# Optimization experiments

Measured on AMD Instinct MI355X. Metric: run time of the kernel, lower is better.

Reference implementation:

```python
import jax, jax.numpy as jnp
import numpy as np

N_HEAD, N_KV, HD, CA_DIM, VE_CH = 16, 4, 64, 32, 12
B, T, C = 4, 1024, 1024
FFN_H = 4 * C
CA_STEPS = 4

def rms_norm(x):
    return x * jax.lax.rsqrt(jnp.mean(x * x, axis=-1, keepdims=True) + 1e-6)

def rope(x, cos, sin):
    d = x.shape[-1] // 2
    x1, x2 = x[..., :d], x[..., d:]
    return jnp.concatenate([x1 * cos + x2 * sin, -x1 * sin + x2 * cos], axis=-1)

def dwconv1d(x_bct, w, pad):  # w: (Cch,1,K) depthwise
    return jax.lax.conv_general_dilated(x_bct, w, (1,), [(pad, pad)],
        feature_group_count=x_bct.shape[1], dimension_numbers=('NCH', 'OIH', 'NCH'))

def dwconv2d(x_bchw, w):  # w: (Cch,1,3,3) depthwise
    return jax.lax.conv_general_dilated(x_bchw, w, (1, 1), [(1, 1), (1, 1)],
        feature_group_count=x_bchw.shape[1], dimension_numbers=('NCHW', 'OIHW', 'NCHW'))

def ca_channel(x, ca_pi, ca_cw, ca_po):
    h = x @ ca_pi.T  # (B,T,CA_DIM)
    h = h + 0.1 * jnp.transpose(dwconv1d(jnp.transpose(h, (0, 2, 1)), ca_cw, 1), (0, 2, 1))
    return jax.nn.gelu(h, approximate=False) @ ca_po.T

def setup_inputs() -> dict:
    key = jax.random.key(0)
    ks = jax.random.split(key, 20)
    s = 0.02
    pos = jnp.arange(T, dtype=jnp.float32)
    inv_freq = 1.0 / (10000.0 ** (jnp.arange(HD // 2, dtype=jnp.float32) / (HD // 2)))
    ang = pos[:, None] * inv_freq[None, :]  # (T, HD/2)
    return {
        'x': jax.random.normal(ks[0], (B, T, C), jnp.float32),
        've': jax.random.normal(ks[1], (B, T, N_KV * HD), jnp.float32),
        'cos': jnp.cos(ang)[None, :, None, :],
        'sin': jnp.sin(ang)[None, :, None, :],
        'prev_attn': jax.random.uniform(ks[2], (B, N_HEAD, T, T), jnp.float32),
        'w_q': s * jax.random.normal(ks[3], (N_HEAD * HD, C), jnp.float32),
        'w_k': s * jax.random.normal(ks[4], (N_KV * HD, C), jnp.float32),
        'w_v': s * jax.random.normal(ks[5], (N_KV * HD, C), jnp.float32),
        'w_o': s * jax.random.normal(ks[6], (C, C), jnp.float32),
        'w_ve_gate': s * jax.random.normal(ks[7], (N_KV, VE_CH), jnp.float32),
        'refine_w': s * jax.random.normal(ks[8], (N_HEAD, 1, 3, 3), jnp.float32),
        'refine_alpha': jnp.float32(0.05),
        'ca_pi': s * jax.random.normal(ks[9], (CA_DIM, C), jnp.float32),
        'ca_cw': s * jax.random.normal(ks[10], (CA_DIM, 1, 3), jnp.float32),
        'ca_po': s * jax.random.normal(ks[11], (C, CA_DIM), jnp.float32),
        'ffn_in': s * jax.random.normal(ks[12], (FFN_H, C), jnp.float32),
        'ffn_cw': s * jax.random.normal(ks[13], (FFN_H, 1, 3), jnp.float32),
        'ffn_out': s * jax.random.normal(ks[14], (C, FFN_H), jnp.float32),
        'ffn_gate': s * jax.random.normal(ks[15], (C, C), jnp.float32),
        'vit_w1': s * jax.random.normal(ks[16], (32, C), jnp.float32),
        'vit_w2': s * jax.random.normal(ks[17], (1, 32), jnp.float32),
    }

def reference(x, ve, cos, sin, prev_attn, w_q, w_k, w_v, w_o, w_ve_gate,
              refine_w, refine_alpha, ca_pi, ca_cw, ca_po,
              ffn_in, ffn_cw, ffn_out, ffn_gate, vit_w1, vit_w2):
    Bx, Tx, Cx = x.shape
    xn = rms_norm(x)
    q = (xn @ w_q.T).reshape(Bx, Tx, N_HEAD, HD)
    k = (xn @ w_k.T).reshape(Bx, Tx, N_KV, HD)
    v = (xn @ w_v.T).reshape(Bx, Tx, N_KV, HD)
    gate = 3.0 * jax.nn.sigmoid(xn[..., :VE_CH] @ w_ve_gate.T)  # (B,T,N_KV)
    v = v + gate[..., None] * ve.reshape(Bx, Tx, N_KV, HD)
    q = rms_norm(rope(q, cos, sin)) * 1.2
    k = rms_norm(rope(k, cos, sin)) * 1.2
    r = N_HEAD // N_KV
    k = jnp.repeat(k, r, axis=2)
    v = jnp.repeat(v, r, axis=2)
    q, k, v = (jnp.transpose(t, (0, 2, 1, 3)) for t in (q, k, v))  # (B,H,T,HD)
    att = jnp.einsum('bhqd,bhkd->bhqk', q, k) * (1.0 / np.sqrt(HD))
    att = att + refine_alpha * dwconv2d(prev_attn[:, :, :Tx, :Tx], refine_w)
    cmask = jnp.tril(jnp.ones((Tx, Tx), bool))
    att = jnp.where(cmask, att, -jnp.inf)
    aw = jax.nn.softmax(att, axis=-1)
    y = jnp.einsum('bhqk,bhkd->bhqd', aw, v)
    attn_out = jnp.transpose(y, (0, 2, 1, 3)).reshape(Bx, Tx, Cx) @ w_o.T
    # ca_mode='both': gate the attention output
    ca1 = ca_channel(x, ca_pi, ca_cw, ca_po)
    x1 = x + attn_out * (1.0 + 0.1 * jnp.tanh(ca1))
    # CAFFN
    xm = rms_norm(x1)
    h = jnp.square(jax.nn.relu(xm @ ffn_in.T))  # (B,T,FFN_H)
    ht = jnp.transpose(h, (0, 2, 1))
    for _ in range(CA_STEPS):
        ht = ht + 0.1 * dwconv1d(ht, ffn_cw, 1)
    h = jnp.transpose(ht, (0, 2, 1))
    mlp = (h @ ffn_out.T) * jax.nn.sigmoid(xm @ ffn_gate.T)
    ca2 = ca_channel(x1, ca_pi, ca_cw, ca_po)
    mlp = mlp * (1.0 + 0.1 * jnp.tanh(ca2))
    # vitality gating: MLP -> sigmoid, then avg_pool1d(k=5, pad=2, zero-counted)
    vit = jax.nn.sigmoid(jax.nn.gelu(x1 @ vit_w1.T, approximate=False) @ vit_w2.T)[..., 0]  # (B,T)
    vp = jnp.pad(vit, ((0, 0), (2, 2)))
    vs = sum(vp[:, i:i + Tx] for i in range(5)) / 5.0
    vit = 0.7 * vit + 0.3 * vs
    vit = jnp.where(vit > 0.3, vit, vit * 0.1)
    return x1 + mlp * vit[..., None]
```

## Files before the change

kernel.cpp:

```cpp
#include <hip/hip_runtime.h>

#define BB 4
#define TT 1024
#define CC 1024
#define NH 16
#define NKV 4
#define HD 64
#define FFNH 4096
#define CAD 32
#define TQ 64
#define TK 64

typedef short bf16x8 __attribute__((ext_vector_type(8)));
typedef float f32x4  __attribute__((ext_vector_type(4)));

#define AS1 __attribute__((address_space(1)))
#define AS3 __attribute__((address_space(3)))

__device__ __forceinline__ float sigf(float x){ return 1.f/(1.f+__expf(-x)); }
__device__ __forceinline__ float geluf(float x){ return 0.5f*x*(1.f+erff(x*0.70710678118654752f)); }

__device__ __forceinline__ unsigned short f2bf(float f){
  unsigned int u = __float_as_uint(f);
  u += 0x7fffu + ((u >> 16) & 1u);
  return (unsigned short)(u >> 16);
}
__device__ __forceinline__ float bf2f(unsigned short h){
  return __uint_as_float(((unsigned int)h) << 16);
}

__global__ __launch_bounds__(256) void rmsnorm_pair_k(const float* __restrict__ x,
    unsigned short* __restrict__ oh, unsigned short* __restrict__ ol){
  int row = blockIdx.x;
  const float* xr = x + (size_t)row * CC;
  float v[4]; float ss = 0.f;
  #pragma unroll
  for (int i = 0; i < 4; i++){ v[i] = xr[threadIdx.x + 256*i]; ss += v[i]*v[i]; }
  #pragma unroll
  for (int off = 1; off < 64; off <<= 1) ss += __shfl_xor(ss, off);
  __shared__ float red[4];
  if ((threadIdx.x & 63) == 0) red[threadIdx.x >> 6] = ss;
  __syncthreads();
  float tot = red[0]+red[1]+red[2]+red[3];
  float rs = rsqrtf(tot * (1.f/CC) + 1e-6f);
  size_t base = (size_t)row * CC;
  #pragma unroll
  for (int i = 0; i < 4; i++){
    float r = v[i]*rs;
    unsigned short h = f2bf(r);
    oh[base + threadIdx.x + 256*i] = h;
    ol[base + threadIdx.x + 256*i] = f2bf(r - bf2f(h));
  }
}

__global__ __launch_bounds__(256) void split_k(const float* __restrict__ in,
    unsigned short* __restrict__ hi, unsigned short* __restrict__ lo, int n4){
  int i = blockIdx.x*256 + threadIdx.x;
  if (i >= n4) return;
  float4 v = ((const float4*)in)[i];
  unsigned short h0 = f2bf(v.x), h1 = f2bf(v.y), h2v = f2bf(v.z), h3 = f2bf(v.w);
  ushort4 hv = { h0, h1, h2v, h3 };
  ushort4 lv = { f2bf(v.x - bf2f(h0)), f2bf(v.y - bf2f(h1)),
                 f2bf(v.z - bf2f(h2v)), f2bf(v.w - bf2f(h3)) };
  ((ushort4*)hi)[i] = hv;
  ((ushort4*)lo)[i] = lv;
}

template<int EPI>
__global__ __launch_bounds__(256) void gemm3_k(
    const unsigned short* __restrict__ Ah, const unsigned short* __restrict__ Al,
    const unsigned short* __restrict__ Wh, const unsigned short* __restrict__ Wl,
    float* __restrict__ C, int M, int N, int K)
{
  __shared__ unsigned short AhS[128*32];
  __shared__ unsigned short AlS[128*32];
  __shared__ unsigned short WhS[128*32];
  __shared__ unsigned short WlS[128*32];
  int tid  = threadIdx.x;
  int lane = tid & 63, wave = tid >> 6;
  int wr = wave >> 1, wc = wave & 1;
  int m0 = blockIdx.y << 7, n0 = blockIdx.x << 7;
  int lr = lane & 15, lc = lane >> 4;

  int offA[4], offB[4];
  #pragma unroll
  for (int m = 0; m < 4; m++){
    int row = wr*64 + m*16 + lr;
    offA[m] = row*64 + ((lc ^ ((row >> 1) & 3)) << 4);
  }
  #pragma unroll
  for (int n = 0; n < 4; n++){
    int row = wc*64 + n*16 + lr;
    offB[n] = row*64 + ((lc ^ ((row >> 1) & 3)) << 4);
  }

  f32x4 acc[4][4] = {};

  for (int k0 = 0; k0 < K; k0 += 32){
    __syncthreads();
    {
      const unsigned short* srcs[4] = { Ah, Al, Wh, Wl };
      unsigned short* dsts[4] = { AhS, AlS, WhS, WlS };
      int rb[4] = { m0, m0, n0, n0 };
      #pragma unroll
      for (int tle = 0; tle < 4; tle++){
        #pragma unroll
        for (int i = 0; i < 2; i++){
          int s = i*256 + tid;
          int row = s >> 2;
          int c = (s & 3) ^ ((row >> 1) & 3);
          const unsigned short* gp = srcs[tle] + (size_t)(rb[tle] + row)*K + (k0 + c*8);
          unsigned short* lp = dsts[tle] + i*2048 + wave*512;
          __builtin_amdgcn_global_load_lds((const AS1 void*)gp, (AS3 void*)lp, 16, 0, 0);
        }
      }
    }
    __syncthreads();

    bf16x8 ah[4], al[4], bh[4], bl[4];
    #pragma unroll
    for (int m = 0; m < 4; m++){
      ah[m] = *(const bf16x8*)((const char*)AhS + offA[m]);
      al[m] = *(const bf16x8*)((const char*)AlS + offA[m]);
    }
    #pragma unroll
    for (int n = 0; n < 4; n++){
      bh[n] = *(const bf16x8*)((const char*)WhS + offB[n]);
      bl[n] = *(const bf16x8*)((const char*)WlS + offB[n]);
    }
    #pragma unroll
    for (int m = 0; m < 4; m++){
      #pragma unroll
      for (int n = 0; n < 4; n++){
        acc[m][n] = __builtin_amdgcn_mfma_f32_16x16x32_bf16(al[m], bh[n], acc[m][n], 0, 0, 0);
        acc[m][n] = __builtin_amdgcn_mfma_f32_16x16x32_bf16(ah[m], bl[n], acc[m][n], 0, 0, 0);
        acc[m][n] = __builtin_amdgcn_mfma_f32_16x16x32_bf16(ah[m], bh[n], acc[m][n], 0, 0, 0);
      }
    }
  }

  #pragma unroll
  for (int m = 0; m < 4; m++){
    int r0 = m0 + wr*64 + m*16 + lc*4;
    #pragma unroll
    for (int n = 0; n < 4; n++){
      int col = n0 + wc*64 + n*16 + lr;
      #pragma unroll
      for (int r = 0; r < 4; r++){
        float z = acc[m][n][r];
        if (EPI == 1){ z = fmaxf(z, 0.f); z = z*z; }
        C[(size_t)(r0 + r)*N + col] = z;
      }
    }
  }
}

__global__ __launch_bounds__(64) void rope_rms_k(float* __restrict__ q,
    const float* __restrict__ cs, const float* __restrict__ sn, int nh){
  int idx = blockIdx.x;
  int t = (idx / nh) & (TT-1);
  float* qp = q + (size_t)idx * HD;
  int d = threadIdx.x;
  int dl = d & 31;
  float c = cs[t*32 + dl], s = sn[t*32 + dl];
  float v0 = qp[d];
  float vp = qp[(d < 32) ? d + 32 : d - 32];
  float r = (d < 32) ? (v0*c + vp*s) : (v0*c - vp*s);
  float ss = r*r;
  #pragma unroll
  for (int off = 1; off < 64; off <<= 1) ss += __shfl_xor(ss, off);
  float rs = rsqrtf(ss*(1.f/HD) + 1e-6f) * 1.2f;
  qp[d] = r*rs;
}

__global__ __launch_bounds__(256) void gatev_k(float* __restrict__ v,
    const unsigned short* __restrict__ xnh, const unsigned short* __restrict__ xnl,
    const float* __restrict__ ve, const float* __restrict__ wg){
  int bt = blockIdx.x;
  int tid = threadIdx.x;
  int kv = tid >> 6;
  float s = 0.f;
  #pragma unroll
  for (int j = 0; j < 12; j++){
    float xv = bf2f(xnh[(size_t)bt*CC + j]) + bf2f(xnl[(size_t)bt*CC + j]);
    s += xv*wg[kv*12+j];
  }
  float gate = 3.f * sigf(s);
  size_t i = (size_t)bt*(NKV*HD) + tid;
  v[i] += gate * ve[i];
}

__global__ __launch_bounds__(256) void fattn_k(
    const float* __restrict__ q, const float* __restrict__ k, const float* __restrict__ v,
    const float* __restrict__ pa, const float* __restrict__ rw,
    const float* __restrict__ alphap,
    unsigned short* __restrict__ yh, unsigned short* __restrict__ yl)
{
  int qt = blockIdx.x;
  int h  = blockIdx.y;
  int b  = blockIdx.z;
  int kv = h >> 2;
  int t0 = qt * TQ;
  int tid = threadIdx.x;
  int lane = tid & 63, w = tid >> 6;
  int dl = lane & 15, gq = lane >> 4;

  __shared__ __align__(16) unsigned short Kh[4096], Kl[4096];
  __shared__ __align__(16) unsigned short Vh[64][68];
  __shared__ __align__(16) unsigned short SBs[66*68];
  __shared__ __align__(16) unsigned short Ph[4][1024];

  bf16x8 qfh[2], qfl[2];
  {
    const float* qrow = q + (((size_t)(b*TT + t0 + 16*w + dl))*NH + h)*HD;
    #pragma unroll
    for (int ks = 0; ks < 2; ks++){
      float4 a = *(const float4*)(qrow + (gq+4*ks)*8);
      float4 bq = *(const float4*)(qrow + (gq+4*ks)*8 + 4);
      float vv[8] = {a.x,a.y,a.z,a.w,bq.x,bq.y,bq.z,bq.w};
      #pragma unroll
      for (int i = 0; i < 8; i++){
        unsigned short hv = f2bf(vv[i]);
        qfh[ks][i] = (short)hv;
        qfl[ks][i] = (short)f2bf(vv[i] - bf2f(hv));
      }
    }
  }

  float alpha = *alphap;
  float w9[9];
  #pragma unroll
  for (int j = 0; j < 9; j++) w9[j] = rw[h*9+j]*alpha;

  float m_i = -1e30f, l_i = 0.f;
  f32x4 acc_o[4] = {};
  int ql = 16*w + dl;

  for (int kt = 0; kt <= qt; kt++){
    int k0 = kt*TK;
    __syncthreads();
    #pragma unroll
    for (int it = 0; it < 4; it++){
      int s = it*256 + tid;
      int r = s >> 4, d4 = (s & 15) << 2;
      const float* kp = k + (((size_t)(b*TT + k0 + r))*NKV + kv)*HD + d4;
      float4 val = *(const float4*)kp;
      ushort4 hv = { f2bf(val.x), f2bf(val.y), f2bf(val.z), f2bf(val.w) };
      ushort4 lv = { f2bf(val.x - bf2f(hv.x)), f2bf(val.y - bf2f(hv.y)),
                     f2bf(val.z - bf2f(hv.z)), f2bf(val.w - bf2f(hv.w)) };
      int idx = r*64 + (((d4 >> 3) ^ (r & 7)) << 3) + (d4 & 7);
      *(ushort4*)&Kh[idx] = hv;
      *(ushort4*)&Kl[idx] = lv;
      const float* vp = v + (((size_t)(b*TT + k0 + r))*NKV + kv)*HD + d4;
      float4 vval = *(const float4*)vp;
      ushort4 vh4 = { f2bf(vval.x), f2bf(vval.y), f2bf(vval.z), f2bf(vval.w) };
      *(ushort4*)&Vh[r][d4] = vh4;
    }
    #pragma unroll
    for (int it = 0; it < 4; it++){
      int e = it*256 + tid;
      int r = e >> 4, c4 = (e & 15) << 2;
      const float* pp = pa + ((size_t)(b*NH + h)*TT + (t0 + r))*TT + (k0 + c4);
      float4 pv = *(const float4*)pp;
      unsigned short* sp = &SBs[(r+1)*68 + (c4+1)];
      sp[0] = f2bf(pv.x); sp[1] = f2bf(pv.y); sp[2] = f2bf(pv.z); sp[3] = f2bf(pv.w);
    }
    for (int e = tid; e < 260; e += 256){
      int li, lj;
      if (e < 132){ li = (e < 66) ? 0 : 65; lj = (e < 66) ? e : e - 66; }
      else { int idx = e - 132; li = 1 + (idx & 63); lj = (idx >> 6) ? 65 : 0; }
      int gr = t0 - 1 + li, gc = k0 - 1 + lj;
      float pv = 0.f;
      if (gr >= 0 && gr < TT && gc >= 0 && gc < TT)
        pv = pa[((size_t)(b*NH + h)*TT + gr)*TT + gc];
      SBs[li*68 + lj] = f2bf(pv);
    }
    __syncthreads();

    f32x4 acc_s[4] = {};
    __builtin_amdgcn_s_setprio(1);
    #pragma unroll
    for (int ks = 0; ks < 2; ks++){
      #pragma unroll
      for (int kf = 0; kf < 4; kf++){
        int row = 16*kf + dl;
        int idx = row*64 + (((gq + 4*ks) ^ (row & 7)) << 3);
        bf16x8 kh_ = *(const bf16x8*)&Kh[idx];
        bf16x8 kl_ = *(const bf16x8*)&Kl[idx];
        acc_s[kf] = __builtin_amdgcn_mfma_f32_16x16x32_bf16(kl_, qfh[ks], acc_s[kf], 0, 0, 0);
        acc_s[kf] = __builtin_amdgcn_mfma_f32_16x16x32_bf16(kh_, qfl[ks], acc_s[kf], 0, 0, 0);
        acc_s[kf] = __builtin_amdgcn_mfma_f32_16x16x32_bf16(kh_, qfh[ks], acc_s[kf], 0, 0, 0);
      }
    }
    __builtin_amdgcn_s_setprio(0);

    #pragma unroll
    for (int kf = 0; kf < 4; kf++){
      int kb = 16*kf + 4*gq;
      float cv0=0.f, cv1=0.f, cv2=0.f, cv3=0.f;
      #pragma unroll
      for (int dy = 0; dy < 3; dy++){
        const unsigned short* rp = &SBs[(ql + dy)*68 + kb];
        float u0 = bf2f(rp[0]), u1 = bf2f(rp[1]), u2 = bf2f(rp[2]),
              u3 = bf2f(rp[3]), u4 = bf2f(rp[4]), u5 = bf2f(rp[5]);
        float wa = w9[dy*3+0], wb = w9[dy*3+1], wcq = w9[dy*3+2];
        cv0 += u0*wa + u1*wb + u2*wcq;
        cv1 += u1*wa + u2*wb + u3*wcq;
        cv2 += u2*wa + u3*wb + u4*wcq;
        cv3 += u3*wa + u4*wb + u5*wcq;
      }
      int grow = t0 + ql;
      float s0 = acc_s[kf][0]*0.125f + cv0; if (k0 + kb + 0 > grow) s0 = -1e30f;
      float s1 = acc_s[kf][1]*0.125f + cv1; if (k0 + kb + 1 > grow) s1 = -1e30f;
      float s2 = acc_s[kf][2]*0.125f + cv2; if (k0 + kb + 2 > grow) s2 = -1e30f;
      float s3 = acc_s[kf][3]*0.125f + cv3; if (k0 + kb + 3 > grow) s3 = -1e30f;
      acc_s[kf][0] = s0; acc_s[kf][1] = s1; acc_s[kf][2] = s2; acc_s[kf][3] = s3;
    }

    float rm = -1e30f;
    #pragma unroll
    for (int kf = 0; kf < 4; kf++){
      rm = fmaxf(rm, fmaxf(fmaxf(acc_s[kf][0], acc_s[kf][1]),
                           fmaxf(acc_s[kf][2], acc_s[kf][3])));
    }
    rm = fmaxf(rm, __shfl_xor(rm, 16));
    rm = fmaxf(rm, __shfl_xor(rm, 32));
    float mn = fmaxf(m_i, rm);
    float sc = __expf(m_i - mn);
    m_i = mn;
    float rs = 0.f;
    #pragma unroll
    for (int kf = 0; kf < 4; kf++){
      float p0 = __expf(acc_s[kf][0] - mn);
      float p1 = __expf(acc_s[kf][1] - mn);
      float p2 = __expf(acc_s[kf][2] - mn);
      float p3 = __expf(acc_s[kf][3] - mn);
      rs += p0 + p1 + p2 + p3;
      ushort4 hv = { f2bf(p0), f2bf(p1), f2bf(p2), f2bf(p3) };
      int kbl = 16*kf + 4*gq;
      int idx = dl*64 + ((((kbl >> 3)) ^ (dl & 7)) << 3) + (kbl & 7);
      *(ushort4*)&Ph[w][idx] = hv;
    }
    rs += __shfl_xor(rs, 16);
    rs += __shfl_xor(rs, 32);
    l_i = l_i*sc + rs;

    float scR0 = __shfl(sc, gq*4 + 0);
    float scR1 = __shfl(sc, gq*4 + 1);
    float scR2 = __shfl(sc, gq*4 + 2);
    float scR3 = __shfl(sc, gq*4 + 3);
    #pragma unroll
    for (int nf = 0; nf < 4; nf++){
      acc_o[nf][0] *= scR0; acc_o[nf][1] *= scR1;
      acc_o[nf][2] *= scR2; acc_o[nf][3] *= scR3;
    }

    #pragma unroll
    for (int ks = 0; ks < 2; ks++){
      int idxp = dl*64 + (((gq + 4*ks) ^ (dl & 7)) << 3);
      bf16x8 pfh = *(const bf16x8*)&Ph[w][idxp];
      __builtin_amdgcn_s_setprio(1);
      #pragma unroll
      for (int nf = 0; nf < 4; nf++){
        bf16x8 vh_;
        #pragma unroll
        for (int i = 0; i < 8; i++)
          vh_[i] = (short)Vh[ks*32 + gq*8 + i][16*nf + dl];
        acc_o[nf] = __builtin_amdgcn_mfma_f32_16x16x32_bf16(pfh, vh_, acc_o[nf], 0, 0, 0);
      }
      __builtin_amdgcn_s_setprio(0);
    }
  }

  float li0 = __shfl(l_i, gq*4 + 0);
  float li1 = __shfl(l_i, gq*4 + 1);
  float li2 = __shfl(l_i, gq*4 + 2);
  float li3 = __shfl(l_i, gq*4 + 3);
  float inv0 = 1.f/li0, inv1 = 1.f/li1, inv2 = 1.f/li2, inv3 = 1.f/li3;
  #pragma unroll
  for (int nf = 0; nf < 4; nf++){
    int dcol = 16*nf + dl;
    #pragma unroll
    for (int reg = 0; reg < 4; reg++){
      float invv = (reg == 0) ? inv0 : (reg == 1) ? inv1 : (reg == 2) ? inv2 : inv3;
      float val = acc_o[nf][reg] * invv;
      size_t bix = (((size_t)(b*TT + t0 + 16*w + gq*4 + reg))*NH + h)*HD + dcol;
      unsigned short hv = f2bf(val);
      yh[bix] = hv;
      yl[bix] = f2bf(val - bf2f(hv));
    }
  }
}

__global__ __launch_bounds__(256) void cain_k(const float* __restrict__ x,
    const float* __restrict__ pi, float* __restrict__ out){
  int bt = blockIdx.x;
  __shared__ float xs[CC];
  __shared__ float pr[8][33];
  for (int i = threadIdx.x; i < CC; i += 256) xs[i] = x[(size_t)bt*CC + i];
  __syncthreads();
  int d = threadIdx.x & 31, sl = threadIdx.x >> 5;
  const float* pip = pi + (size_t)d*CC + sl*128;
  float s = 0.f;
  #pragma unroll 8
  for (int i = 0; i < 128; i++) s += xs[sl*128+i]*pip[i];
  pr[sl][d] = s;
  __syncthreads();
  if (threadIdx.x < 32){
    float tot = 0.f;
    #pragma unroll
    for (int j = 0; j < 8; j++) tot += pr[j][threadIdx.x];
    out[(size_t)bt*CAD + threadIdx.x] = tot;
  }
}

__global__ __launch_bounds__(256) void caconv_k(const float* __restrict__ hin,
    const float* __restrict__ cw, float* __restrict__ gout){
  int i = blockIdx.x*256 + threadIdx.x;
  int d = i & 31;
  int bt = i >> 5;
  int t = bt & (TT-1);
  float cc = hin[i];
  float hm = (t > 0)      ? hin[i-32] : 0.f;
  float hp = (t < TT-1)   ? hin[i+32] : 0.f;
  float hc = cc + 0.1f*(hm*cw[d*3] + cc*cw[d*3+1] + hp*cw[d*3+2]);
  gout[i] = geluf(hc);
}

__global__ __launch_bounds__(256) void caout_k(const float* __restrict__ g,
    const float* __restrict__ po, float* __restrict__ out){
  int bt = blockIdx.x;
  __shared__ float gs[CAD];
  if (threadIdx.x < CAD) gs[threadIdx.x] = g[(size_t)bt*CAD + threadIdx.x];
  __syncthreads();
  for (int c = threadIdx.x; c < CC; c += 256){
    const float* pp = po + (size_t)c*CAD;
    float s = 0.f;
    #pragma unroll
    for (int d2 = 0; d2 < CAD; d2++) s += gs[d2]*pp[d2];
    out[(size_t)bt*CC + c] = s;
  }
}

__global__ __launch_bounds__(256) void x1_k(const float* __restrict__ x,
    const float* __restrict__ ao, const float* __restrict__ ca1, float* __restrict__ x1){
  size_t i = (size_t)blockIdx.x*256 + threadIdx.x;
  x1[i] = x[i] + ao[i] * (1.f + 0.1f*tanhf(ca1[i]));
}

__global__ __launch_bounds__(256) void ffnconv4_k(const float* __restrict__ hin,
    const float* __restrict__ cw, unsigned short* __restrict__ hh, unsigned short* __restrict__ hl){
  int c  = blockIdx.x*256 + threadIdx.x;
  int ta = blockIdx.y*64;
  int b  = blockIdx.z;
  float w0 = cw[c*3+0], w1 = cw[c*3+1], w2 = cw[c*3+2];
  size_t base = (size_t)b*TT*FFNH + c;
  float i0=0.f,i1=0.f,i2=0.f;
  float a0=0.f,a1=0.f,a2=0.f;
  float b0=0.f,b1=0.f,b2=0.f;
  float c0=0.f,c1=0.f,c2=0.f;
  for (int t = ta-4; t <= ta+67; t++){
    float iv = 0.f;
    if (t >= 0 && t < TT) iv = hin[base + (size_t)t*FFNH];
    i0 = i1; i1 = i2; i2 = iv;
    float s1 = i1 + 0.1f*(i0*w0 + i1*w1 + i2*w2);
    if (t-1 < 0 || t-1 >= TT) s1 = 0.f;
    a0 = a1; a1 = a2; a2 = s1;
    float s2 = a1 + 0.1f*(a0*w0 + a1*w1 + a2*w2);
    if (t-2 < 0 || t-2 >= TT) s2 = 0.f;
    b0 = b1; b1 = b2; b2 = s2;
    float s3 = b1 + 0.1f*(b0*w0 + b1*w1 + b2*w2);
    if (t-3 < 0 || t-3 >= TT) s3 = 0.f;
    c0 = c1; c1 = c2; c2 = s3;
    float s4 = c1 + 0.1f*(c0*w0 + c1*w1 + c2*w2);
    int t4 = t-4;
    if (t4 >= ta){
      size_t oix = base + (size_t)t4*FFNH;
      unsigned short hv = f2bf(s4);
      hh[oix] = hv;
      hl[oix] = f2bf(s4 - bf2f(hv));
    }
  }
}

__global__ __launch_bounds__(256) void vit_k(const float* __restrict__ x1,
    const float* __restrict__ w1, const float* __restrict__ w2,
    float* __restrict__ vout){
  int bt = blockIdx.x;
  __shared__ float xs[CC];
  __shared__ float pr[8][33];
  __shared__ float g32[32];
  for (int i = threadIdx.x; i < CC; i += 256) xs[i] = x1[(size_t)bt*CC + i];
  __syncthreads();
  int d = threadIdx.x & 31, sl = threadIdx.x >> 5;
  const float* wp = w1 + (size_t)d*CC + sl*128;
  float s = 0.f;
  #pragma unroll 8
  for (int i = 0; i < 128; i++) s += xs[sl*128+i]*wp[i];
  pr[sl][d] = s;
  __syncthreads();
  if (threadIdx.x < 32){
    float tot = 0.f;
    #pragma unroll
    for (int j = 0; j < 8; j++) tot += pr[j][threadIdx.x];
    g32[threadIdx.x] = geluf(tot);
  }
  __syncthreads();
  if (threadIdx.x == 0){
    float s2 = 0.f;
    #pragma unroll
    for (int d2 = 0; d2 < 32; d2++) s2 += g32[d2]*w2[d2];
    vout[bt] = sigf(s2);
  }
}

__global__ __launch_bounds__(256) void vitsm_k(const float* __restrict__ vin, float* __restrict__ vout){
  int i = blockIdx.x*256 + threadIdx.x;
  int t = i & (TT-1), b = i >> 10;
  float s = 0.f;
  #pragma unroll
  for (int dd = -2; dd <= 2; dd++){
    int tt = t + dd;
    if (tt >= 0 && tt < TT) s += vin[(b << 10) + tt];
  }
  s *= 0.2f;
  float vv = 0.7f*vin[i] + 0.3f*s;
  vout[i] = (vv > 0.3f) ? vv : 0.1f*vv;
}

__global__ __launch_bounds__(256) void final_k(const float* __restrict__ x1,
    const float* __restrict__ mlpraw, const float* __restrict__ g,
    const float* __restrict__ ca2, const float* __restrict__ vsm,
    float* __restrict__ out){
  size_t i = (size_t)blockIdx.x*256 + threadIdx.x;
  size_t bt = i >> 10;
  float mlp = mlpraw[i] * sigf(g[i]) * (1.f + 0.1f*tanhf(ca2[i]));
  out[i] = x1[i] + mlp * vsm[bt];
}

extern "C" void kernel_launch(void* const* d_in, const int* in_sizes, int n_in,
                              void* d_out, int out_size, void* d_ws, size_t ws_size,
                              hipStream_t stream) {
  (void)in_sizes; (void)n_in; (void)out_size; (void)ws_size;
  const float* x     = (const float*)d_in[0];
  const float* ve    = (const float*)d_in[1];
  const float* cs    = (const float*)d_in[2];
  const float* sn    = (const float*)d_in[3];
  const float* pa    = (const float*)d_in[4];
  const float* w_q   = (const float*)d_in[5];
  const float* w_k   = (const float*)d_in[6];
  const float* w_v   = (const float*)d_in[7];
  const float* w_o   = (const float*)d_in[8];
  const float* w_vg  = (const float*)d_in[9];
  const float* rfw   = (const float*)d_in[10];
  const float* ralp  = (const float*)d_in[11];
  const float* capi  = (const float*)d_in[12];
  const float* cacw  = (const float*)d_in[13];
  const float* capo  = (const float*)d_in[14];
  const float* ffin  = (const float*)d_in[15];
  const float* ffcw  = (const float*)d_in[16];
  const float* ffout = (const float*)d_in[17];
  const float* ffgt  = (const float*)d_in[18];
  const float* vw1   = (const float*)d_in[19];
  const float* vw2   = (const float*)d_in[20];

  const size_t M4  = (size_t)BB*TT*CC;
  const size_t MB1 = 1ull << 20;
  char* WSB = (char*)d_ws;

  unsigned short* xnh = (unsigned short*)WSB;
  unsigned short* xnl = xnh + M4;
  float* ca1 = (float*)WSB;
  float* qb  = (float*)(WSB + 16*MB1);
  float* kb  = (float*)(WSB + 32*MB1);
  unsigned short* ffgp = (unsigned short*)(WSB + 32*MB1);
  float* vb  = (float*)(WSB + 36*MB1);
  float* cah = (float*)(WSB + 36*MB1);
  float* cag = cah + (size_t)BB*TT*CAD;
  float* vtb = cag + (size_t)BB*TT*CAD;
  float* vsm = vtb + (size_t)BB*TT;
  float* ao  = (float*)(WSB + 40*MB1);
  float* x1b = (float*)(WSB + 56*MB1);
  unsigned short* yh = (unsigned short*)x1b;
  unsigned short* yl = yh + M4;
  float* hb  = (float*)(WSB + 72*MB1);
  float* h2  = (float*)(WSB + 136*MB1);
  unsigned short* hh = (unsigned short*)h2;
  unsigned short* hl = hh + 4*M4;
  unsigned short* wqp = (unsigned short*)(WSB + 136*MB1);
  unsigned short* wkp = (unsigned short*)(WSB + 140*MB1);
  unsigned short* wvp = (unsigned short*)(WSB + 141*MB1);
  unsigned short* wop = (unsigned short*)(WSB + 142*MB1);
  float* ca2 = h2;
  unsigned short* ffip = (unsigned short*)(WSB + 200*MB1);
  unsigned short* ffop = (unsigned short*)(WSB + 216*MB1);

  const int BT = BB*TT;
  const int WQN = NH*HD*CC;
  const int WKN = NKV*HD*CC;

  split_k<<<WQN/1024, 256, 0, stream>>>(w_q, wqp, wqp + WQN, WQN/4);
  split_k<<<WKN/1024, 256, 0, stream>>>(w_k, wkp, wkp + WKN, WKN/4);
  split_k<<<WKN/1024, 256, 0, stream>>>(w_v, wvp, wvp + WKN, WKN/4);
  split_k<<<WQN/1024, 256, 0, stream>>>(w_o, wop, wop + WQN, WQN/4);
  split_k<<<M4/1024, 256, 0, stream>>>(ffin, ffip, ffip + M4, (int)(M4/4));
  split_k<<<M4/1024, 256, 0, stream>>>(ffout, ffop, ffop + M4, (int)(M4/4));

  rmsnorm_pair_k<<<BT, 256, 0, stream>>>(x, xnh, xnl);
  gemm3_k<0><<<dim3(8, 32), 256, 0, stream>>>(xnh, xnl, wqp, wqp + WQN, qb, BT, 1024, 1024);
  gemm3_k<0><<<dim3(2, 32), 256, 0, stream>>>(xnh, xnl, wkp, wkp + WKN, kb, BT, 256, 1024);
  gemm3_k<0><<<dim3(2, 32), 256, 0, stream>>>(xnh, xnl, wvp, wvp + WKN, vb, BT, 256, 1024);
  rope_rms_k<<<BT*NH, 64, 0, stream>>>(qb, cs, sn, NH);
  rope_rms_k<<<BT*NKV, 64, 0, stream>>>(kb, cs, sn, NKV);
  gatev_k<<<BT, 256, 0, stream>>>(vb, xnh, xnl, ve, w_vg);
  fattn_k<<<dim3(TT/TQ, NH, BB), 256, 0, stream>>>(qb, kb, vb, pa, rfw, ralp, yh, yl);
  gemm3_k<0><<<dim3(8, 32), 256, 0, stream>>>(yh, yl, wop, wop + WQN, ao, BT, 1024, 1024);
  split_k<<<WQN/1024, 256, 0, stream>>>(ffgt, ffgp, ffgp + WQN, WQN/4);
  cain_k<<<BT, 256, 0, stream>>>(x, capi, cah);
  caconv_k<<<BT*CAD/256, 256, 0, stream>>>(cah, cacw, cag);
  caout_k<<<BT, 256, 0, stream>>>(cag, capo, ca1);
  x1_k<<<BT*CC/256, 256, 0, stream>>>(x, ao, ca1, x1b);
  rmsnorm_pair_k<<<BT, 256, 0, stream>>>(x1b, xnh, xnl);
  gemm3_k<1><<<dim3(32, 32), 256, 0, stream>>>(xnh, xnl, ffip, ffip + M4, hb, BT, FFNH, 1024);
  ffnconv4_k<<<dim3(FFNH/256, TT/64, BB), 256, 0, stream>>>(hb, ffcw, hh, hl);
  gemm3_k<0><<<dim3(8, 32), 256, 0, stream>>>(xnh, xnl, ffgp, ffgp + WQN, qb, BT, 1024, 1024);
  gemm3_k<0><<<dim3(8, 32), 256, 0, stream>>>(hh, hl, ffop, ffop + M4, ao, BT, 1024, FFNH);
  cain_k<<<BT, 256, 0, stream>>>(x1b, capi, cah);
  caconv_k<<<BT*CAD/256, 256, 0, stream>>>(cah, cacw, cag);
  caout_k<<<BT, 256, 0, stream>>>(cag, capo, ca2);
  vit_k<<<BT, 256, 0, stream>>>(x1b, vw1, vw2, vtb);
  vitsm_k<<<BT/256, 256, 0, stream>>>(vtb, vsm);
  final_k<<<BT*CC/256, 256, 0, stream>>>(x1b, ao, qb, ca2, vsm, (float*)d_out);
}
```

Measured before the change: 1.574 ms.

## Add split-K partitioning to under-occupied GEMMs with a separate reduction kernel

The split bf16 GEMM kernel gains a K-chunk parameter and a blockIdx.z partition, so each z-slice writes its own partial output. The Q, K, V, O, gate and FFN-out projections now launch 2–4 K-slices, followed by a new float4 reduction kernel that sums the partials. The aim is to fill more compute units for GEMMs with few output tiles, such as the K/V projections with only 64 blocks and the long-K FFN-out projection. In exchange it costs extra partial-buffer memory traffic, extra kernel launches, and reuses the FFN hidden buffer as scratch for the partials.

Measured after the change: 1.441 ms. 8.4% less time.

```diff
diff --git a/kernel.cpp b/kernel.cpp
--- a/kernel.cpp
+++ b/kernel.cpp
@@ -70,7 +70,7 @@
 __global__ __launch_bounds__(256) void gemm3_k(
     const unsigned short* __restrict__ Ah, const unsigned short* __restrict__ Al,
     const unsigned short* __restrict__ Wh, const unsigned short* __restrict__ Wl,
-    float* __restrict__ C, int M, int N, int K)
+    float* __restrict__ C, int M, int N, int K, int KC)
 {
   __shared__ unsigned short AhS[128*32];
   __shared__ unsigned short AlS[128*32];
@@ -80,6 +80,9 @@
   int lane = tid & 63, wave = tid >> 6;
   int wr = wave >> 1, wc = wave & 1;
   int m0 = blockIdx.y << 7, n0 = blockIdx.x << 7;
+  int z  = blockIdx.z;
+  int kbase = z * KC;
+  float* Cz = C + (size_t)z * M * N;
   int lr = lane & 15, lc = lane >> 4;
 
   int offA[4], offB[4];
@@ -96,7 +99,7 @@
 
   f32x4 acc[4][4] = {};
 
-  for (int k0 = 0; k0 < K; k0 += 32){
+  for (int k0 = kbase; k0 < kbase + KC; k0 += 32){
     __syncthreads();
     {
       const unsigned short* srcs[4] = { Ah, Al, Wh, Wl };
@@ -147,12 +150,23 @@
       int col = n0 + wc*64 + n*16 + lr;
       #pragma unroll
       for (int r = 0; r < 4; r++){
-        float z = acc[m][n][r];
-        if (EPI == 1){ z = fmaxf(z, 0.f); z = z*z; }
-        C[(size_t)(r0 + r)*N + col] = z;
+        float z2 = acc[m][n][r];
+        if (EPI == 1){ z2 = fmaxf(z2, 0.f); z2 = z2*z2; }
+        Cz[(size_t)(r0 + r)*N + col] = z2;
       }
     }
   }
+}
+
+__global__ __launch_bounds__(256) void redsum_k(const float* __restrict__ p,
+    float* __restrict__ o, size_t n, int parts){
+  size_t i = ((size_t)blockIdx.x*256 + threadIdx.x)*4;
+  float4 s = *(const float4*)(p + i);
+  for (int z = 1; z < parts; z++){
+    float4 q = *(const float4*)(p + (size_t)z*n + i);
+    s.x += q.x; s.y += q.y; s.z += q.z; s.w += q.w;
+  }
+  *(float4*)(o + i) = s;
 }
 
 __global__ __launch_bounds__(64) void rope_rms_k(float* __restrict__ q,
@@ -595,6 +609,13 @@
   unsigned short* ffip = (unsigned short*)(WSB + 200*MB1);
   unsigned short* ffop = (unsigned short*)(WSB + 216*MB1);
 
+  float* kpart = hb;
+  float* vpart = hb + 4*M4/4;
+  float* qpart = hb + 8*M4/4;
+  float* opart = hb;
+  float* gpart = hb;
+  float* fpart = hb;
+
   const int BT = BB*TT;
   const int WQN = NH*HD*CC;
   const int WKN = NKV*HD*CC;
@@ -607,24 +628,30 @@
   split_k<<<M4/1024, 256, 0, stream>>>(ffout, ffop, ffop + M4, (int)(M4/4));
 
   rmsnorm_pair_k<<<BT, 256, 0, stream>>>(x, xnh, xnl);
-  gemm3_k<0><<<dim3(8, 32), 256, 0, stream>>>(xnh, xnl, wqp, wqp + WQN, qb, BT, 1024, 1024);
-  gemm3_k<0><<<dim3(2, 32), 256, 0, stream>>>(xnh, xnl, wkp, wkp + WKN, kb, BT, 256, 1024);
-  gemm3_k<0><<<dim3(2, 32), 256, 0, stream>>>(xnh, xnl, wvp, wvp + WKN, vb, BT, 256, 1024);
+  gemm3_k<0><<<dim3(8, 32, 2), 256, 0, stream>>>(xnh, xnl, wqp, wqp + WQN, qpart, BT, 1024, 1024, 512);
+  redsum_k<<<4096, 256, 0, stream>>>(qpart, qb, (size_t)BT*1024, 2);
+  gemm3_k<0><<<dim3(2, 32, 4), 256, 0, stream>>>(xnh, xnl, wkp, wkp + WKN, kpart, BT, 256, 1024, 256);
+  redsum_k<<<1024, 256, 0, stream>>>(kpart, kb, (size_t)BT*256, 4);
+  gemm3_k<0><<<dim3(2, 32, 4), 256, 0, stream>>>(xnh, xnl, wvp, wvp + WKN, vpart, BT, 256, 1024, 256);
+  redsum_k<<<1024, 256, 0, stream>>>(vpart, vb, (size_t)BT*256, 4);
   rope_rms_k<<<BT*NH, 64, 0, stream>>>(qb, cs, sn, NH);
   rope_rms_k<<<BT*NKV, 64, 0, stream>>>(kb, cs, sn, NKV);
   gatev_k<<<BT, 256, 0, stream>>>(vb, xnh, xnl, ve, w_vg);
   fattn_k<<<dim3(TT/TQ, NH, BB), 256, 0, stream>>>(qb, kb, vb, pa, rfw, ralp, yh, yl);
-  gemm3_k<0><<<dim3(8, 32), 256, 0, stream>>>(yh, yl, wop, wop + WQN, ao, BT, 1024, 1024);
+  gemm3_k<0><<<dim3(8, 32, 2), 256, 0, stream>>>(yh, yl, wop, wop + WQN, opart, BT, 1024, 1024, 512);
+  redsum_k<<<4096, 256, 0, stream>>>(opart, ao, (size_t)BT*1024, 2);
   split_k<<<WQN/1024, 256, 0, stream>>>(ffgt, ffgp, ffgp + WQN, WQN/4);
   cain_k<<<BT, 256, 0, stream>>>(x, capi, cah);
   caconv_k<<<BT*CAD/256, 256, 0, stream>>>(cah, cacw, cag);
   caout_k<<<BT, 256, 0, stream>>>(cag, capo, ca1);
   x1_k<<<BT*CC/256, 256, 0, stream>>>(x, ao, ca1, x1b);
   rmsnorm_pair_k<<<BT, 256, 0, stream>>>(x1b, xnh, xnl);
-  gemm3_k<1><<<dim3(32, 32), 256, 0, stream>>>(xnh, xnl, ffip, ffip + M4, hb, BT, FFNH, 1024);
+  gemm3_k<1><<<dim3(32, 32), 256, 0, stream>>>(xnh, xnl, ffip, ffip + M4, hb, BT, FFNH, 1024, 1024);
   ffnconv4_k<<<dim3(FFNH/256, TT/64, BB), 256, 0, stream>>>(hb, ffcw, hh, hl);
-  gemm3_k<0><<<dim3(8, 32), 256, 0, stream>>>(xnh, xnl, ffgp, ffgp + WQN, qb, BT, 1024, 1024);
-  gemm3_k<0><<<dim3(8, 32), 256, 0, stream>>>(hh, hl, ffop, ffop + M4, ao, BT, 1024, FFNH);
+  gemm3_k<0><<<dim3(8, 32, 2), 256, 0, stream>>>(xnh, xnl, ffgp, ffgp + WQN, gpart, BT, 1024, 1024, 512);
+  redsum_k<<<4096, 256, 0, stream>>>(gpart, qb, (size_t)BT*1024, 2);
+  gemm3_k<0><<<dim3(8, 32, 4), 256, 0, stream>>>(hh, hl, ffop, ffop + M4, fpart, BT, 1024, 4096, 1024);
+  redsum_k<<<4096, 256, 0, stream>>>(fpart, ao, (size_t)BT*1024, 4);
   cain_k<<<BT, 256, 0, stream>>>(x1b, capi, cah);
   caconv_k<<<BT*CAD/256, 256, 0, stream>>>(cah, cacw, cag);
   caout_k<<<BT, 256, 0, stream>>>(cag, capo, ca2);
```
